# Kernel optimization log

Measured on AMD Instinct MI355X. Metric: run time of the kernel, lower is better.

The kernel has to match this reference:

```python
import jax, jax.numpy as jnp
import numpy as np

B, N, F = 128, 64, 64          # batch, nodes, node features
FE = [2 * F + 1, 256, 256, 96] # edge MLP: fe_in = 2*node_size + num_ef(=1 dist)
FN = [FE[-1] + F, 256, 64]     # node MLP: fe_out + node_size
ALPHA = 0.2

def _lin(key, fan_in, fan_out):
    kw, kb = jax.random.split(key)
    s = 1.0 / np.sqrt(fan_in)
    return (jax.random.normal(kw, (fan_in, fan_out), jnp.float32) * s,
            jax.random.normal(kb, (fan_out,), jnp.float32) * s)

def setup_inputs() -> dict:
    key = jax.random.key(0)
    ks = jax.random.split(key, 6)
    x = jax.random.normal(ks[0], (B, N, F), jnp.float32)
    fe_W0, fe_b0 = _lin(ks[1], FE[0], FE[1])
    fe_W1, fe_b1 = _lin(ks[2], FE[1], FE[2])
    fe_W2, fe_b2 = _lin(ks[3], FE[2], FE[3])
    fn_W0, fn_b0 = _lin(ks[4], FN[0], FN[1])
    fn_W1, fn_b1 = _lin(ks[5], FN[1], FN[2])
    return {"x": x,
            "fe_W0": fe_W0, "fe_b0": fe_b0, "fe_W1": fe_W1, "fe_b1": fe_b1,
            "fe_W2": fe_W2, "fe_b2": fe_b2,
            "fn_W0": fn_W0, "fn_b0": fn_b0, "fn_W1": fn_W1, "fn_b1": fn_b1}

def _lrelu(v):
    return jax.nn.leaky_relu(v, ALPHA)

def reference(x, fe_W0, fe_b0, fe_W1, fe_b1, fe_W2, fe_b2, fn_W0, fn_b0, fn_W1, fn_b1):
    b, n, f = x.shape
    # fully-connected pairwise edge features: x1[b,i,j]=x[b,i], x2[b,i,j]=x[b,j]
    xi = jnp.broadcast_to(x[:, :, None, :], (b, n, n, f))
    xj = jnp.broadcast_to(x[:, None, :, :], (b, n, n, f))
    diffs = xj - xi
    dists = jnp.linalg.norm(diffs + 1e-12, axis=-1, keepdims=True)  # all_ef distance
    A = jnp.concatenate([xi, xj, dists], axis=-1)                   # [B,N,N,2F+1]
    # edge MLP fe (final_linear=False -> leaky relu after every layer)
    h = _lrelu(A @ fe_W0 + fe_b0)
    h = _lrelu(h @ fe_W1 + fe_b1)
    h = _lrelu(h @ fe_W2 + fe_b2)                                   # [B,N,N,96]
    agg = jnp.sum(h, axis=2)                                        # sum over neighbors j
    y = jnp.concatenate([agg, x], axis=-1)                          # [B,N,160]
    # node MLP fn (final_linear=True -> last layer linear)
    y = _lrelu(y @ fn_W0 + fn_b0)
    y = y @ fn_W1 + fn_b1                                           # [B,N,64]
    return y
```

## Files before the change

kernel.cpp:

```cpp
#include <hip/hip_runtime.h>

#define ALPHA 0.2f

typedef __attribute__((ext_vector_type(8))) short short8;
typedef __attribute__((ext_vector_type(4))) float f32x4;
typedef __attribute__((ext_vector_type(2))) unsigned int u32x2;
typedef __attribute__((ext_vector_type(4))) unsigned int u32x4;

__device__ __forceinline__ short f2bf(float f) {
    unsigned u = __builtin_bit_cast(unsigned, f);
    u += 0x7fffu + ((u >> 16) & 1u);
    return (short)(u >> 16);
}
__device__ __forceinline__ unsigned pack2(float a, float b) {
    unsigned ua = __builtin_bit_cast(unsigned, a) + 0x8000u;
    unsigned ub = __builtin_bit_cast(unsigned, b) + 0x8000u;
    return (ua >> 16) | (ub & 0xffff0000u);
}
__device__ __forceinline__ float bf2f(short s) {
    return __builtin_bit_cast(float, ((unsigned)(unsigned short)s) << 16);
}
__device__ __forceinline__ float lrelu(float v) { return fmaxf(v, ALPHA * v); }

__global__ void prep_kernel(const float* __restrict__ feW0, const float* __restrict__ feW1,
                            const float* __restrict__ feW2, const float* __restrict__ fnW0,
                            const float* __restrict__ fnW1,
                            short* __restrict__ W1F, short* __restrict__ W2F,
                            short* __restrict__ W0uvF,
                            short* __restrict__ Wn0T, short* __restrict__ Wn1T)
{
    const int tid = blockIdx.x * blockDim.x + threadIdx.x;
    const int T = gridDim.x * blockDim.x;
    for (int t = tid; t < 65536; t += T) {
        int e = t & 7, lane = (t >> 3) & 63, ks = (t >> 9) & 7, mt = t >> 12;
        int feat = mt * 16 + (lane & 15), k = ks * 32 + (lane >> 4) * 8 + e;
        W1F[t] = f2bf(feW1[k * 256 + feat]);
    }
    for (int t = tid; t < 32768; t += T) {
        int e = t & 7, lane = (t >> 3) & 63, ks = (t >> 9) & 7, mt = t >> 12;
        int feat = mt * 16 + (lane & 15), k = ks * 32 + (lane >> 4) * 8 + e;
        W2F[t] = f2bf(feat < 96 ? feW2[k * 96 + feat] : 0.f);
    }
    for (int t = tid; t < 32768; t += T) {
        int e = t & 7, lane = (t >> 3) & 63, ks = (t >> 9) & 1, mt = t >> 10;
        int feat = mt * 16 + (lane & 15), k = ks * 32 + (lane >> 4) * 8 + e;
        float val = (feat < 256) ? feW0[k * 256 + feat] : feW0[(64 + k) * 256 + (feat - 256)];
        W0uvF[t] = f2bf(val);
    }
    for (int t = tid; t < 256 * 160; t += T) { int n = t / 160, k = t - n * 160; Wn0T[t] = f2bf(fnW0[k * 256 + n]); }
    for (int t = tid; t < 64 * 256; t += T) { int n = t >> 8, k = t & 255; Wn1T[t] = f2bf(fnW1[k * 64 + n]); }
}

__global__ __launch_bounds__(256, 4)
void uv_kernel(const float* __restrict__ x, const short* __restrict__ W0uvF,
               float* __restrict__ u, float* __restrict__ v)
{
    __shared__ __align__(16) short xb[4096];
    const int tid = threadIdx.x;
    const int lane = tid & 63, wid = tid >> 6;
    const int l15 = lane & 15, lg = lane >> 4;
    const int r0 = blockIdx.x * 64;

    for (int t = tid; t < 4096; t += 256) {
        int row = t >> 6;
        int byte = (t * 2) ^ ((row & 7) << 4);
        *(short*)((char*)xb + byte) = f2bf(x[r0 * 64 + t]);
    }
    __syncthreads();

    #pragma unroll
    for (int pair = 0; pair < 4; ++pair) {
        const int mt0 = wid * 8 + pair * 2;
        f32x4 acc[2][4];
        #pragma unroll
        for (int m = 0; m < 2; ++m)
            #pragma unroll
            for (int nt = 0; nt < 4; ++nt) acc[m][nt] = (f32x4){0.f, 0.f, 0.f, 0.f};
        #pragma unroll
        for (int ks = 0; ks < 2; ++ks) {
            short8 a[2], bf[4];
            #pragma unroll
            for (int m = 0; m < 2; ++m)
                a[m] = *(const short8*)&W0uvF[(((mt0 + m) * 2 + ks) * 64 + lane) * 8];
            #pragma unroll
            for (int nt = 0; nt < 4; ++nt) {
                int row = nt * 16 + l15;
                int byte = (row * 128 + (ks * 32 + lg * 8) * 2) ^ ((row & 7) << 4);
                bf[nt] = *(const short8*)((char*)xb + byte);
            }
            #pragma unroll
            for (int m = 0; m < 2; ++m)
                #pragma unroll
                for (int nt = 0; nt < 4; ++nt)
                    acc[m][nt] = __builtin_amdgcn_mfma_f32_16x16x32_bf16(a[m], bf[nt], acc[m][nt], 0, 0, 0);
        }
        #pragma unroll
        for (int m = 0; m < 2; ++m) {
            int feat0 = (mt0 + m) * 16 + lg * 4;
            #pragma unroll
            for (int nt = 0; nt < 4; ++nt) {
                int R = r0 + nt * 16 + l15;
                float* dst = (feat0 < 256) ? &u[R * 256 + feat0] : &v[R * 256 + (feat0 - 256)];
                *(f32x4*)dst = acc[m][nt];
            }
        }
    }
}

__global__ __launch_bounds__(512, 2)
void edge_kernel(const float* __restrict__ x, const float* __restrict__ feW0,
                 const float* __restrict__ b0v, const float* __restrict__ b1v,
                 const float* __restrict__ b2v,
                 const short* __restrict__ W1F, const short* __restrict__ W2F,
                 const float* __restrict__ u, const float* __restrict__ v,
                 float* __restrict__ agg)
{
    __shared__ __align__(16) char smem[119808];
    char* vb = smem;
    char* h0 = smem + 32768;
    char* h1 = smem + 65536;
    float* ub_f = (float*)(smem + 98304);
    float* wd_f = (float*)(smem + 114688);
    float* dist = (float*)(smem + 115712);
    float* xs   = (float*)(smem + 65536);

    const int tid = threadIdx.x;
    const int lane = tid & 63, wid = tid >> 6;
    const int l15 = lane & 15, lg = lane >> 4;
    const int j8 = tid >> 3, p8 = tid & 7;
    const int b = blockIdx.x >> 2, i0 = (blockIdx.x & 3) * 16;

    short8 a1[2][8];
    #pragma unroll
    for (int m = 0; m < 2; ++m)
        #pragma unroll
        for (int ks = 0; ks < 8; ++ks)
            a1[m][ks] = *(const short8*)&W1F[(((wid * 2 + m) * 8 + ks) * 64 + lane) * 8];
    short8 a2[8];
    #pragma unroll
    for (int ks = 0; ks < 8; ++ks)
        a2[ks] = *(const short8*)&W2F[((wid * 8 + ks) * 64 + lane) * 8];
    f32x4 bb1[2];
    bb1[0] = *(const f32x4*)&b1v[wid * 32 + lg * 4];
    bb1[1] = *(const f32x4*)&b1v[wid * 32 + 16 + lg * 4];
    f32x4 bb2 = (f32x4){0.f, 0.f, 0.f, 0.f};
    if (wid < 6) bb2 = *(const f32x4*)&b2v[wid * 16 + lg * 4];

    {
        const float* xb = x + b * 4096;
        *(f32x4*)&xs[j8 * 68 + p8 * 8]     = *(const f32x4*)&xb[j8 * 64 + p8 * 8];
        *(f32x4*)&xs[j8 * 68 + p8 * 8 + 4] = *(const f32x4*)&xb[j8 * 64 + p8 * 8 + 4];
    }
    {
        const float* gv = v + (b * 64 + j8) * 256;
        #pragma unroll
        for (int e = 0; e < 4; ++e) {
            int c0 = p8 * 32 + e * 8;
            f32x4 v0 = *(const f32x4*)&gv[c0];
            f32x4 v1 = *(const f32x4*)&gv[c0 + 4];
            u32x4 pk;
            pk[0] = pack2(v0[0], v0[1]); pk[1] = pack2(v0[2], v0[3]);
            pk[2] = pack2(v1[0], v1[1]); pk[3] = pack2(v1[2], v1[3]);
            *(u32x4*)(vb + ((j8 * 512 + c0 * 2) ^ ((j8 & 7) << 4))) = pk;
        }
    }
    {
        int ii = tid >> 5, c0 = (tid & 31) * 8;
        const float* gu = u + (b * 64 + i0 + ii) * 256 + c0;
        f32x4 u0 = *(const f32x4*)&gu[0];
        f32x4 u1 = *(const f32x4*)&gu[4];
        u0 += *(const f32x4*)&b0v[c0];
        u1 += *(const f32x4*)&b0v[c0 + 4];
        int q = c0 >> 2;
        *(f32x4*)&ub_f[(ii * 64 + (q ^ (q >> 3))) * 4] = u0;
        *(f32x4*)&ub_f[(ii * 64 + ((q + 1) ^ ((q + 1) >> 3))) * 4] = u1;
    }
    if (tid < 64) {
        f32x4 w0 = *(const f32x4*)&feW0[128 * 256 + tid * 4];
        *(f32x4*)&wd_f[(tid ^ (tid >> 3)) * 4] = w0;
    }
    __syncthreads();

    {
        f32x4 xj0 = *(const f32x4*)&xs[j8 * 68 + p8 * 8];
        f32x4 xj1 = *(const f32x4*)&xs[j8 * 68 + p8 * 8 + 4];
        #pragma unroll
        for (int ii = 0; ii < 16; ++ii) {
            const float* xi = &xs[(i0 + ii) * 68 + p8 * 8];
            f32x4 xi0 = *(const f32x4*)&xi[0];
            f32x4 xi1 = *(const f32x4*)&xi[4];
            float ss = 0.f;
            #pragma unroll
            for (int r = 0; r < 4; ++r) {
                float d0 = xj0[r] - xi0[r] + 1e-12f;
                float d1 = xj1[r] - xi1[r] + 1e-12f;
                ss += d0 * d0 + d1 * d1;
            }
            ss += __shfl_xor(ss, 1); ss += __shfl_xor(ss, 2); ss += __shfl_xor(ss, 4);
            if (p8 == 0) dist[ii * 64 + j8] = sqrtf(ss);
        }
    }
    __syncthreads();

    #define BUILD(ii_) do { \
        float dj = dist[(ii_) * 64 + j8]; \
        _Pragma("unroll") \
        for (int e = 0; e < 4; ++e) { \
            int c0 = p8 * 32 + e * 8; \
            int q0 = p8 * 8 + e * 2; \
            short8 vr = *(const short8*)(vb + ((j8 * 512 + c0 * 2) ^ ((j8 & 7) << 4))); \
            f32x4 uu0 = *(const f32x4*)&ub_f[((ii_) * 64 + (q0 ^ p8)) * 4]; \
            f32x4 uu1 = *(const f32x4*)&ub_f[((ii_) * 64 + ((q0 + 1) ^ p8)) * 4]; \
            f32x4 ww0 = *(const f32x4*)&wd_f[(q0 ^ p8) * 4]; \
            f32x4 ww1 = *(const f32x4*)&wd_f[((q0 + 1) ^ p8) * 4]; \
            float t0 = lrelu(uu0[0] + bf2f(vr[0]) + dj * ww0[0]); \
            float t1 = lrelu(uu0[1] + bf2f(vr[1]) + dj * ww0[1]); \
            float t2 = lrelu(uu0[2] + bf2f(vr[2]) + dj * ww0[2]); \
            float t3 = lrelu(uu0[3] + bf2f(vr[3]) + dj * ww0[3]); \
            float t4 = lrelu(uu1[0] + bf2f(vr[4]) + dj * ww1[0]); \
            float t5 = lrelu(uu1[1] + bf2f(vr[5]) + dj * ww1[1]); \
            float t6 = lrelu(uu1[2] + bf2f(vr[6]) + dj * ww1[2]); \
            float t7 = lrelu(uu1[3] + bf2f(vr[7]) + dj * ww1[3]); \
            u32x4 pk; \
            pk[0] = pack2(t0, t1); pk[1] = pack2(t2, t3); \
            pk[2] = pack2(t4, t5); pk[3] = pack2(t6, t7); \
            *(u32x4*)(h0 + ((j8 * 512 + c0 * 2) ^ ((j8 & 7) << 4))) = pk; \
        } \
    } while (0)

    BUILD(0);
    __syncthreads();

    float* aggrow = agg + (b * 64 + i0) * 96;
    for (int ii = 0; ii < 16; ++ii) {
        {
            f32x4 acc[2][4];
            #pragma unroll
            for (int m = 0; m < 2; ++m)
                #pragma unroll
                for (int nt = 0; nt < 4; ++nt) acc[m][nt] = (f32x4){0.f, 0.f, 0.f, 0.f};
            #pragma unroll
            for (int ks = 0; ks < 8; ++ks) {
                short8 bfr[4];
                #pragma unroll
                for (int nt = 0; nt < 4; ++nt) {
                    int j = nt * 16 + l15;
                    bfr[nt] = *(const short8*)(h0 + ((j * 512 + (ks * 32 + lg * 8) * 2) ^ ((j & 7) << 4)));
                }
                #pragma unroll
                for (int m = 0; m < 2; ++m)
                    #pragma unroll
                    for (int nt = 0; nt < 4; ++nt)
                        acc[m][nt] = __builtin_amdgcn_mfma_f32_16x16x32_bf16(a1[m][ks], bfr[nt], acc[m][nt], 0, 0, 0);
            }
            #pragma unroll
            for (int m = 0; m < 2; ++m) {
                int f0 = wid * 32 + m * 16 + lg * 4;
                #pragma unroll
                for (int nt = 0; nt < 4; ++nt) {
                    int j = nt * 16 + l15;
                    float q0 = lrelu(acc[m][nt][0] + bb1[m][0]);
                    float q1 = lrelu(acc[m][nt][1] + bb1[m][1]);
                    float q2 = lrelu(acc[m][nt][2] + bb1[m][2]);
                    float q3 = lrelu(acc[m][nt][3] + bb1[m][3]);
                    u32x2 pv; pv[0] = pack2(q0, q1); pv[1] = pack2(q2, q3);
                    *(u32x2*)(h1 + ((j * 512 + f0 * 2) ^ ((j & 7) << 4))) = pv;
                }
            }
        }
        __syncthreads();
        if (ii < 15) BUILD(ii + 1);
        if (wid < 6) {
            f32x4 acc2[4];
            #pragma unroll
            for (int nt = 0; nt < 4; ++nt) acc2[nt] = (f32x4){0.f, 0.f, 0.f, 0.f};
            #pragma unroll
            for (int ks = 0; ks < 8; ++ks) {
                #pragma unroll
                for (int nt = 0; nt < 4; ++nt) {
                    int j = nt * 16 + l15;
                    short8 bfr = *(const short8*)(h1 + ((j * 512 + (ks * 32 + lg * 8) * 2) ^ ((j & 7) << 4)));
                    acc2[nt] = __builtin_amdgcn_mfma_f32_16x16x32_bf16(a2[ks], bfr, acc2[nt], 0, 0, 0);
                }
            }
            f32x4 s = (f32x4){0.f, 0.f, 0.f, 0.f};
            #pragma unroll
            for (int nt = 0; nt < 4; ++nt)
                #pragma unroll
                for (int r = 0; r < 4; ++r)
                    s[r] += lrelu(acc2[nt][r] + bb2[r]);
            #pragma unroll
            for (int r = 0; r < 4; ++r) {
                float t = s[r];
                t += __shfl_xor(t, 1); t += __shfl_xor(t, 2);
                t += __shfl_xor(t, 4); t += __shfl_xor(t, 8);
                s[r] = t;
            }
            if (l15 == 0) *(f32x4*)&aggrow[ii * 96 + wid * 16 + lg * 4] = s;
        }
        __syncthreads();
    }
    #undef BUILD
}

__global__ __launch_bounds__(256, 2)
void node_kernel(const float* __restrict__ x, const float* __restrict__ agg,
                 const short* __restrict__ Wn0T, const short* __restrict__ Wn1T,
                 const float* __restrict__ bn0, const float* __restrict__ bn1,
                 float* __restrict__ out)
{
    __shared__ short A2[64 * 168];
    __shared__ short H[64 * 264];
    const int tid = threadIdx.x;
    const int lane = tid & 63, wid = tid >> 6;
    const int l15 = lane & 15, lg = lane >> 4;
    const int r0 = blockIdx.x * 64;

    for (int t = tid; t < 64 * 160; t += 256) {
        int j = t / 160, c = t - j * 160;
        float vv = (c < 96) ? agg[(r0 + j) * 96 + c] : x[(r0 + j) * 64 + (c - 96)];
        A2[j * 168 + c] = f2bf(vv);
    }
    __syncthreads();

    {
        f32x4 acc[4][4];
        #pragma unroll
        for (int mt = 0; mt < 4; ++mt)
            #pragma unroll
            for (int nt = 0; nt < 4; ++nt) acc[mt][nt] = (f32x4){0.f, 0.f, 0.f, 0.f};
        const int n0 = wid * 64;
        #pragma unroll
        for (int ks = 0; ks < 5; ++ks) {
            const int k0 = ks * 32 + lg * 8;
            short8 a[4], bf[4];
            #pragma unroll
            for (int mt = 0; mt < 4; ++mt)
                a[mt] = *reinterpret_cast<const short8*>(&A2[(mt * 16 + l15) * 168 + k0]);
            #pragma unroll
            for (int nt = 0; nt < 4; ++nt)
                bf[nt] = *reinterpret_cast<const short8*>(&Wn0T[(n0 + nt * 16 + l15) * 160 + k0]);
            #pragma unroll
            for (int mt = 0; mt < 4; ++mt)
                #pragma unroll
                for (int nt = 0; nt < 4; ++nt)
                    acc[mt][nt] = __builtin_amdgcn_mfma_f32_16x16x32_bf16(a[mt], bf[nt], acc[mt][nt], 0, 0, 0);
        }
        #pragma unroll
        for (int nt = 0; nt < 4; ++nt) {
            const int col = n0 + nt * 16 + l15;
            const float bv = bn0[col];
            #pragma unroll
            for (int mt = 0; mt < 4; ++mt)
                #pragma unroll
                for (int r = 0; r < 4; ++r)
                    H[(mt * 16 + lg * 4 + r) * 264 + col] = f2bf(lrelu(acc[mt][nt][r] + bv));
        }
    }
    __syncthreads();

    {
        f32x4 acc[4];
        #pragma unroll
        for (int mt = 0; mt < 4; ++mt) acc[mt] = (f32x4){0.f, 0.f, 0.f, 0.f};
        #pragma unroll
        for (int ks = 0; ks < 8; ++ks) {
            const int k0 = ks * 32 + lg * 8;
            short8 bf = *reinterpret_cast<const short8*>(&Wn1T[(wid * 16 + l15) * 256 + k0]);
            #pragma unroll
            for (int mt = 0; mt < 4; ++mt) {
                short8 a = *reinterpret_cast<const short8*>(&H[(mt * 16 + l15) * 264 + k0]);
                acc[mt] = __builtin_amdgcn_mfma_f32_16x16x32_bf16(a, bf, acc[mt], 0, 0, 0);
            }
        }
        const int col = wid * 16 + l15;
        const float bv = bn1[col];
        #pragma unroll
        for (int mt = 0; mt < 4; ++mt)
            #pragma unroll
            for (int r = 0; r < 4; ++r)
                out[(r0 + mt * 16 + lg * 4 + r) * 64 + col] = acc[mt][r] + bv;
    }
}

extern "C" void kernel_launch(void* const* d_in, const int* in_sizes, int n_in,
                              void* d_out, int out_size, void* d_ws, size_t ws_size,
                              hipStream_t stream) {
    (void)in_sizes; (void)n_in; (void)out_size; (void)ws_size;
    const float* x    = (const float*)d_in[0];
    const float* feW0 = (const float*)d_in[1];
    const float* feb0 = (const float*)d_in[2];
    const float* feW1 = (const float*)d_in[3];
    const float* feb1 = (const float*)d_in[4];
    const float* feW2 = (const float*)d_in[5];
    const float* feb2 = (const float*)d_in[6];
    const float* fnW0 = (const float*)d_in[7];
    const float* fnb0 = (const float*)d_in[8];
    const float* fnW1 = (const float*)d_in[9];
    const float* fnb1 = (const float*)d_in[10];

    char* ws = (char*)d_ws;
    short* W1F   = (short*)(ws + 0);
    short* W2F   = (short*)(ws + 131072);
    short* W0uvF = (short*)(ws + 196608);
    short* Wn0T  = (short*)(ws + 262144);
    short* Wn1T  = (short*)(ws + 344064);
    float* agg   = (float*)(ws + 376832);
    float* u     = (float*)(ws + 3522560);
    float* v     = (float*)(ws + 11911168);

    hipLaunchKernelGGL(prep_kernel, dim3(64), dim3(256), 0, stream,
                       feW0, feW1, feW2, fnW0, fnW1, W1F, W2F, W0uvF, Wn0T, Wn1T);
    hipLaunchKernelGGL(uv_kernel, dim3(128), dim3(256), 0, stream,
                       x, W0uvF, u, v);
    hipLaunchKernelGGL(edge_kernel, dim3(512), dim3(512), 0, stream,
                       x, feW0, feb0, feb1, feb2, W1F, W2F, u, v, agg);
    hipLaunchKernelGGL(node_kernel, dim3(128), dim3(256), 0, stream,
                       x, agg, Wn0T, Wn1T, fnb0, fnb1, (float*)d_out);
}
```

Measured before the change: 163.4 us.

## Re-tile edge MLP waves as 4 feature groups by 2 neighbor halves

Changes how the 8 waves split the edge-MLP layer-1 and layer-2 GEMMs. Each wave now covers 64 output features by 32 neighbors, where before it covered 32 features by all 64 neighbors, and all 8 waves now work on layer 2 instead of only 6. Layer-2 partial neighbor sums are combined through a small shared buffer, and each aggregated row is written one iteration late. Biases move to shared memory, and s_setprio is raised around the MFMA bursts. The aim is better wave balance and higher B-operand reuse in layer 2, at the cost of more A-fragment registers, some shared memory, and wasted MFMA work on the zero-padded features 96-127.

```diff
diff --git a/kernel.cpp b/kernel.cpp
--- a/kernel.cpp
+++ b/kernel.cpp
@@ -115,36 +115,37 @@
                  const float* __restrict__ u, const float* __restrict__ v,
                  float* __restrict__ agg)
 {
-    __shared__ __align__(16) char smem[119808];
+    __shared__ __align__(16) char smem[122368];
     char* vb = smem;
     char* h0 = smem + 32768;
     char* h1 = smem + 65536;
     float* ub_f = (float*)(smem + 98304);
     float* wd_f = (float*)(smem + 114688);
     float* dist = (float*)(smem + 115712);
+    float* part = (float*)(smem + 119808);
+    float* bb1s = (float*)(smem + 120832);
+    float* bb2s = (float*)(smem + 121856);
     float* xs   = (float*)(smem + 65536);
 
     const int tid = threadIdx.x;
     const int lane = tid & 63, wid = tid >> 6;
     const int l15 = lane & 15, lg = lane >> 4;
     const int j8 = tid >> 3, p8 = tid & 7;
+    const int fw = wid & 3, jh = wid >> 2;
     const int b = blockIdx.x >> 2, i0 = (blockIdx.x & 3) * 16;
 
-    short8 a1[2][8];
+    short8 a1[4][8];
+    #pragma unroll
+    for (int m = 0; m < 4; ++m)
+        #pragma unroll
+        for (int ks = 0; ks < 8; ++ks)
+            a1[m][ks] = *(const short8*)&W1F[(((fw * 4 + m) * 8 + ks) * 64 + lane) * 8];
+    short8 a2[2][8];
     #pragma unroll
     for (int m = 0; m < 2; ++m)
         #pragma unroll
         for (int ks = 0; ks < 8; ++ks)
-            a1[m][ks] = *(const short8*)&W1F[(((wid * 2 + m) * 8 + ks) * 64 + lane) * 8];
-    short8 a2[8];
-    #pragma unroll
-    for (int ks = 0; ks < 8; ++ks)
-        a2[ks] = *(const short8*)&W2F[((wid * 8 + ks) * 64 + lane) * 8];
-    f32x4 bb1[2];
-    bb1[0] = *(const f32x4*)&b1v[wid * 32 + lg * 4];
-    bb1[1] = *(const f32x4*)&b1v[wid * 32 + 16 + lg * 4];
-    f32x4 bb2 = (f32x4){0.f, 0.f, 0.f, 0.f};
-    if (wid < 6) bb2 = *(const f32x4*)&b2v[wid * 16 + lg * 4];
+            a2[m][ks] = *(const short8*)&W2F[(((fw * 2 + m) * 8 + ks) * 64 + lane) * 8];
 
     {
         const float* xb = x + b * 4096;
@@ -172,13 +173,15 @@
         u0 += *(const f32x4*)&b0v[c0];
         u1 += *(const f32x4*)&b0v[c0 + 4];
         int q = c0 >> 2;
-        *(f32x4*)&ub_f[(ii * 64 + (q ^ (q >> 3))) * 4] = u0;
-        *(f32x4*)&ub_f[(ii * 64 + ((q + 1) ^ ((q + 1) >> 3))) * 4] = u1;
+        *(f32x4*)&ub_f[(q ^ (q >> 3)) * 4 + ii * 256] = u0;
+        *(f32x4*)&ub_f[((q + 1) ^ ((q + 1) >> 3)) * 4 + ii * 256] = u1;
     }
     if (tid < 64) {
         f32x4 w0 = *(const f32x4*)&feW0[128 * 256 + tid * 4];
         *(f32x4*)&wd_f[(tid ^ (tid >> 3)) * 4] = w0;
     }
+    if (tid < 256) bb1s[tid] = b1v[tid];
+    if (tid >= 256 && tid < 384) bb2s[tid - 256] = (tid - 256 < 96) ? b2v[tid - 256] : 0.f;
     __syncthreads();
 
     {
@@ -209,8 +212,8 @@
             int c0 = p8 * 32 + e * 8; \
             int q0 = p8 * 8 + e * 2; \
             short8 vr = *(const short8*)(vb + ((j8 * 512 + c0 * 2) ^ ((j8 & 7) << 4))); \
-            f32x4 uu0 = *(const f32x4*)&ub_f[((ii_) * 64 + (q0 ^ p8)) * 4]; \
-            f32x4 uu1 = *(const f32x4*)&ub_f[((ii_) * 64 + ((q0 + 1) ^ p8)) * 4]; \
+            f32x4 uu0 = *(const f32x4*)&ub_f[(q0 ^ p8) * 4 + (ii_) * 256]; \
+            f32x4 uu1 = *(const f32x4*)&ub_f[((q0 + 1) ^ p8) * 4 + (ii_) * 256]; \
             f32x4 ww0 = *(const f32x4*)&wd_f[(q0 ^ p8) * 4]; \
             f32x4 ww1 = *(const f32x4*)&wd_f[((q0 + 1) ^ p8) * 4]; \
             float t0 = lrelu(uu0[0] + bf2f(vr[0]) + dj * ww0[0]); \
@@ -233,36 +236,42 @@
 
     float* aggrow = agg + (b * 64 + i0) * 96;
     for (int ii = 0; ii < 16; ++ii) {
+        if (ii > 0 && tid < 96)
+            aggrow[(ii - 1) * 96 + tid] = part[tid] + part[128 + tid];
         {
-            f32x4 acc[2][4];
-            #pragma unroll
-            for (int m = 0; m < 2; ++m)
-                #pragma unroll
-                for (int nt = 0; nt < 4; ++nt) acc[m][nt] = (f32x4){0.f, 0.f, 0.f, 0.f};
+            f32x4 acc[4][2];
+            #pragma unroll
+            for (int m = 0; m < 4; ++m) {
+                acc[m][0] = (f32x4){0.f, 0.f, 0.f, 0.f};
+                acc[m][1] = (f32x4){0.f, 0.f, 0.f, 0.f};
+            }
             #pragma unroll
             for (int ks = 0; ks < 8; ++ks) {
-                short8 bfr[4];
-                #pragma unroll
-                for (int nt = 0; nt < 4; ++nt) {
-                    int j = nt * 16 + l15;
+                short8 bfr[2];
+                #pragma unroll
+                for (int nt = 0; nt < 2; ++nt) {
+                    int j = jh * 32 + nt * 16 + l15;
                     bfr[nt] = *(const short8*)(h0 + ((j * 512 + (ks * 32 + lg * 8) * 2) ^ ((j & 7) << 4)));
                 }
-                #pragma unroll
-                for (int m = 0; m < 2; ++m)
+                __builtin_amdgcn_s_setprio(1);
+                #pragma unroll
+                for (int m = 0; m < 4; ++m)
                     #pragma unroll
-                    for (int nt = 0; nt < 4; ++nt)
+                    for (int nt = 0; nt < 2; ++nt)
                         acc[m][nt] = __builtin_amdgcn_mfma_f32_16x16x32_bf16(a1[m][ks], bfr[nt], acc[m][nt], 0, 0, 0);
-            }
-            #pragma unroll
-            for (int m = 0; m < 2; ++m) {
-                int f0 = wid * 32 + m * 16 + lg * 4;
-                #pragma unroll
-                for (int nt = 0; nt < 4; ++nt) {
-                    int j = nt * 16 + l15;
-                    float q0 = lrelu(acc[m][nt][0] + bb1[m][0]);
-                    float q1 = lrelu(acc[m][nt][1] + bb1[m][1]);
-                    float q2 = lrelu(acc[m][nt][2] + bb1[m][2]);
-                    float q3 = lrelu(acc[m][nt][3] + bb1[m][3]);
+                __builtin_amdgcn_s_setprio(0);
+            }
+            #pragma unroll
+            for (int m = 0; m < 4; ++m) {
+                int f0 = fw * 64 + m * 16 + lg * 4;
+                f32x4 bb = *(const f32x4*)&bb1s[f0];
+                #pragma unroll
+                for (int nt = 0; nt < 2; ++nt) {
+                    int j = jh * 32 + nt * 16 + l15;
+                    float q0 = lrelu(acc[m][nt][0] + bb[0]);
+                    float q1 = lrelu(acc[m][nt][1] + bb[1]);
+                    float q2 = lrelu(acc[m][nt][2] + bb[2]);
+                    float q3 = lrelu(acc[m][nt][3] + bb[3]);
                     u32x2 pv; pv[0] = pack2(q0, q1); pv[1] = pack2(q2, q3);
                     *(u32x2*)(h1 + ((j * 512 + f0 * 2) ^ ((j & 7) << 4))) = pv;
                 }
@@ -270,36 +279,48 @@
         }
         __syncthreads();
         if (ii < 15) BUILD(ii + 1);
-        if (wid < 6) {
-            f32x4 acc2[4];
-            #pragma unroll
-            for (int nt = 0; nt < 4; ++nt) acc2[nt] = (f32x4){0.f, 0.f, 0.f, 0.f};
+        {
+            f32x4 acc2[2][2];
+            acc2[0][0] = (f32x4){0.f,0.f,0.f,0.f}; acc2[0][1] = (f32x4){0.f,0.f,0.f,0.f};
+            acc2[1][0] = (f32x4){0.f,0.f,0.f,0.f}; acc2[1][1] = (f32x4){0.f,0.f,0.f,0.f};
             #pragma unroll
             for (int ks = 0; ks < 8; ++ks) {
-                #pragma unroll
-                for (int nt = 0; nt < 4; ++nt) {
-                    int j = nt * 16 + l15;
-                    short8 bfr = *(const short8*)(h1 + ((j * 512 + (ks * 32 + lg * 8) * 2) ^ ((j & 7) << 4)));
-                    acc2[nt] = __builtin_amdgcn_mfma_f32_16x16x32_bf16(a2[ks], bfr, acc2[nt], 0, 0, 0);
+                short8 bfr[2];
+                #pragma unroll
+                for (int nt = 0; nt < 2; ++nt) {
+                    int j = jh * 32 + nt * 16 + l15;
+                    bfr[nt] = *(const short8*)(h1 + ((j * 512 + (ks * 32 + lg * 8) * 2) ^ ((j & 7) << 4)));
                 }
-            }
-            f32x4 s = (f32x4){0.f, 0.f, 0.f, 0.f};
-            #pragma unroll
-            for (int nt = 0; nt < 4; ++nt)
+                __builtin_amdgcn_s_setprio(1);
+                #pragma unroll
+                for (int m = 0; m < 2; ++m)
+                    #pragma unroll
+                    for (int nt = 0; nt < 2; ++nt)
+                        acc2[m][nt] = __builtin_amdgcn_mfma_f32_16x16x32_bf16(a2[m][ks], bfr[nt], acc2[m][nt], 0, 0, 0);
+                __builtin_amdgcn_s_setprio(0);
+            }
+            #pragma unroll
+            for (int m = 0; m < 2; ++m) {
+                int f0 = fw * 32 + m * 16 + lg * 4;
+                f32x4 bb = *(const f32x4*)&bb2s[f0];
+                f32x4 s;
                 #pragma unroll
                 for (int r = 0; r < 4; ++r)
-                    s[r] += lrelu(acc2[nt][r] + bb2[r]);
-            #pragma unroll
-            for (int r = 0; r < 4; ++r) {
-                float t = s[r];
-                t += __shfl_xor(t, 1); t += __shfl_xor(t, 2);
-                t += __shfl_xor(t, 4); t += __shfl_xor(t, 8);
-                s[r] = t;
-            }
-            if (l15 == 0) *(f32x4*)&aggrow[ii * 96 + wid * 16 + lg * 4] = s;
+                    s[r] = lrelu(acc2[m][0][r] + bb[r]) + lrelu(acc2[m][1][r] + bb[r]);
+                #pragma unroll
+                for (int r = 0; r < 4; ++r) {
+                    float t = s[r];
+                    t += __shfl_xor(t, 1); t += __shfl_xor(t, 2);
+                    t += __shfl_xor(t, 4); t += __shfl_xor(t, 8);
+                    s[r] = t;
+                }
+                if (l15 == 0) *(f32x4*)&part[jh * 128 + f0] = s;
+            }
         }
         __syncthreads();
     }
+    if (tid < 96)
+        aggrow[15 * 96 + tid] = part[tid] + part[128 + tid];
     #undef BUILD
 }
 
```

Measured after the change: 230.8 us. 41.3% more time.

## Shrink edge kernel LDS by reading v from global and storing u as bf16

Applied to the files above, without the earlier changes.

The per-block v tile is no longer staged in LDS as bf16; BUILD now reads v directly from global memory (likely L2/L1 resident) in fp32. The u+bias rows are stored as packed bf16 instead of fp32, and the layer-1/2 biases move from registers into LDS to ease register pressure. Shared memory drops from about 117 KB to about 78 KB, which may allow more blocks per CU. In exchange, every BUILD step issues repeated global loads of v, and u is rounded to bf16 earlier.

```diff
diff --git a/kernel.cpp b/kernel.cpp
--- a/kernel.cpp
+++ b/kernel.cpp
@@ -115,20 +115,22 @@
                  const float* __restrict__ u, const float* __restrict__ v,
                  float* __restrict__ agg)
 {
-    __shared__ __align__(16) char smem[119808];
-    char* vb = smem;
-    char* h0 = smem + 32768;
-    char* h1 = smem + 65536;
-    float* ub_f = (float*)(smem + 98304);
-    float* wd_f = (float*)(smem + 114688);
-    float* dist = (float*)(smem + 115712);
-    float* xs   = (float*)(smem + 65536);
+    __shared__ __align__(16) char smem[80384];
+    char* h0 = smem;
+    char* h1 = smem + 32768;
+    short* ub_b = (short*)(smem + 65536);
+    float* wd_f = (float*)(smem + 73728);
+    float* dist = (float*)(smem + 74752);
+    float* bb1s = (float*)(smem + 78848);
+    float* bb2s = (float*)(smem + 79872);
+    float* xs   = (float*)(smem + 32768);
 
     const int tid = threadIdx.x;
     const int lane = tid & 63, wid = tid >> 6;
     const int l15 = lane & 15, lg = lane >> 4;
     const int j8 = tid >> 3, p8 = tid & 7;
     const int b = blockIdx.x >> 2, i0 = (blockIdx.x & 3) * 16;
+    const float* vbase = v + (size_t)b * 64 * 256;
 
     short8 a1[2][8];
     #pragma unroll
@@ -139,12 +141,7 @@
     short8 a2[8];
     #pragma unroll
     for (int ks = 0; ks < 8; ++ks)
-        a2[ks] = *(const short8*)&W2F[((wid * 8 + ks) * 64 + lane) * 8];
-    f32x4 bb1[2];
-    bb1[0] = *(const f32x4*)&b1v[wid * 32 + lg * 4];
-    bb1[1] = *(const f32x4*)&b1v[wid * 32 + 16 + lg * 4];
-    f32x4 bb2 = (f32x4){0.f, 0.f, 0.f, 0.f};
-    if (wid < 6) bb2 = *(const f32x4*)&b2v[wid * 16 + lg * 4];
+        a2[ks] = *(const short8*)&W2F[((min(wid, 5) * 8 + ks) * 64 + lane) * 8];
 
     {
         const float* xb = x + b * 4096;
@@ -152,33 +149,22 @@
         *(f32x4*)&xs[j8 * 68 + p8 * 8 + 4] = *(const f32x4*)&xb[j8 * 64 + p8 * 8 + 4];
     }
     {
-        const float* gv = v + (b * 64 + j8) * 256;
-        #pragma unroll
-        for (int e = 0; e < 4; ++e) {
-            int c0 = p8 * 32 + e * 8;
-            f32x4 v0 = *(const f32x4*)&gv[c0];
-            f32x4 v1 = *(const f32x4*)&gv[c0 + 4];
-            u32x4 pk;
-            pk[0] = pack2(v0[0], v0[1]); pk[1] = pack2(v0[2], v0[3]);
-            pk[2] = pack2(v1[0], v1[1]); pk[3] = pack2(v1[2], v1[3]);
-            *(u32x4*)(vb + ((j8 * 512 + c0 * 2) ^ ((j8 & 7) << 4))) = pk;
-        }
-    }
-    {
         int ii = tid >> 5, c0 = (tid & 31) * 8;
-        const float* gu = u + (b * 64 + i0 + ii) * 256 + c0;
-        f32x4 u0 = *(const f32x4*)&gu[0];
-        f32x4 u1 = *(const f32x4*)&gu[4];
+        f32x4 u0 = *(const f32x4*)&u[(b * 64 + i0 + ii) * 256 + c0];
+        f32x4 u1 = *(const f32x4*)&u[(b * 64 + i0 + ii) * 256 + c0 + 4];
         u0 += *(const f32x4*)&b0v[c0];
         u1 += *(const f32x4*)&b0v[c0 + 4];
-        int q = c0 >> 2;
-        *(f32x4*)&ub_f[(ii * 64 + (q ^ (q >> 3))) * 4] = u0;
-        *(f32x4*)&ub_f[(ii * 64 + ((q + 1) ^ ((q + 1) >> 3))) * 4] = u1;
+        u32x4 pk;
+        pk[0] = pack2(u0[0], u0[1]); pk[1] = pack2(u0[2], u0[3]);
+        pk[2] = pack2(u1[0], u1[1]); pk[3] = pack2(u1[2], u1[3]);
+        *(u32x4*)&ub_b[ii * 256 + c0] = pk;
     }
     if (tid < 64) {
         f32x4 w0 = *(const f32x4*)&feW0[128 * 256 + tid * 4];
-        *(f32x4*)&wd_f[(tid ^ (tid >> 3)) * 4] = w0;
-    }
+        *(f32x4*)&wd_f[tid * 4] = w0;
+    }
+    if (tid < 256) bb1s[tid] = b1v[tid];
+    else if (tid < 352) bb2s[tid - 256] = b2v[tid - 256];
     __syncthreads();
 
     {
@@ -204,23 +190,23 @@
 
     #define BUILD(ii_) do { \
         float dj = dist[(ii_) * 64 + j8]; \
+        const float* gv = vbase + j8 * 256 + p8 * 32; \
         _Pragma("unroll") \
         for (int e = 0; e < 4; ++e) { \
             int c0 = p8 * 32 + e * 8; \
-            int q0 = p8 * 8 + e * 2; \
-            short8 vr = *(const short8*)(vb + ((j8 * 512 + c0 * 2) ^ ((j8 & 7) << 4))); \
-            f32x4 uu0 = *(const f32x4*)&ub_f[((ii_) * 64 + (q0 ^ p8)) * 4]; \
-            f32x4 uu1 = *(const f32x4*)&ub_f[((ii_) * 64 + ((q0 + 1) ^ p8)) * 4]; \
-            f32x4 ww0 = *(const f32x4*)&wd_f[(q0 ^ p8) * 4]; \
-            f32x4 ww1 = *(const f32x4*)&wd_f[((q0 + 1) ^ p8) * 4]; \
-            float t0 = lrelu(uu0[0] + bf2f(vr[0]) + dj * ww0[0]); \
-            float t1 = lrelu(uu0[1] + bf2f(vr[1]) + dj * ww0[1]); \
-            float t2 = lrelu(uu0[2] + bf2f(vr[2]) + dj * ww0[2]); \
-            float t3 = lrelu(uu0[3] + bf2f(vr[3]) + dj * ww0[3]); \
-            float t4 = lrelu(uu1[0] + bf2f(vr[4]) + dj * ww1[0]); \
-            float t5 = lrelu(uu1[1] + bf2f(vr[5]) + dj * ww1[1]); \
-            float t6 = lrelu(uu1[2] + bf2f(vr[6]) + dj * ww1[2]); \
-            float t7 = lrelu(uu1[3] + bf2f(vr[7]) + dj * ww1[3]); \
+            f32x4 va = *(const f32x4*)&gv[e * 8]; \
+            f32x4 vb4 = *(const f32x4*)&gv[e * 8 + 4]; \
+            short8 ur = *(const short8*)&ub_b[(ii_) * 256 + c0]; \
+            f32x4 ww0 = *(const f32x4*)&wd_f[c0]; \
+            f32x4 ww1 = *(const f32x4*)&wd_f[c0 + 4]; \
+            float t0 = lrelu(bf2f(ur[0]) + va[0] + dj * ww0[0]); \
+            float t1 = lrelu(bf2f(ur[1]) + va[1] + dj * ww0[1]); \
+            float t2 = lrelu(bf2f(ur[2]) + va[2] + dj * ww0[2]); \
+            float t3 = lrelu(bf2f(ur[3]) + va[3] + dj * ww0[3]); \
+            float t4 = lrelu(bf2f(ur[4]) + vb4[0] + dj * ww1[0]); \
+            float t5 = lrelu(bf2f(ur[5]) + vb4[1] + dj * ww1[1]); \
+            float t6 = lrelu(bf2f(ur[6]) + vb4[2] + dj * ww1[2]); \
+            float t7 = lrelu(bf2f(ur[7]) + vb4[3] + dj * ww1[3]); \
             u32x4 pk; \
             pk[0] = pack2(t0, t1); pk[1] = pack2(t2, t3); \
             pk[2] = pack2(t4, t5); pk[3] = pack2(t6, t7); \
@@ -256,13 +242,14 @@
             #pragma unroll
             for (int m = 0; m < 2; ++m) {
                 int f0 = wid * 32 + m * 16 + lg * 4;
+                f32x4 bb = *(const f32x4*)&bb1s[f0];
                 #pragma unroll
                 for (int nt = 0; nt < 4; ++nt) {
                     int j = nt * 16 + l15;
-                    float q0 = lrelu(acc[m][nt][0] + bb1[m][0]);
-                    float q1 = lrelu(acc[m][nt][1] + bb1[m][1]);
-                    float q2 = lrelu(acc[m][nt][2] + bb1[m][2]);
-                    float q3 = lrelu(acc[m][nt][3] + bb1[m][3]);
+                    float q0 = lrelu(acc[m][nt][0] + bb[0]);
+                    float q1 = lrelu(acc[m][nt][1] + bb[1]);
+                    float q2 = lrelu(acc[m][nt][2] + bb[2]);
+                    float q3 = lrelu(acc[m][nt][3] + bb[3]);
                     u32x2 pv; pv[0] = pack2(q0, q1); pv[1] = pack2(q2, q3);
                     *(u32x2*)(h1 + ((j * 512 + f0 * 2) ^ ((j & 7) << 4))) = pv;
                 }
@@ -283,12 +270,14 @@
                     acc2[nt] = __builtin_amdgcn_mfma_f32_16x16x32_bf16(a2[ks], bfr, acc2[nt], 0, 0, 0);
                 }
             }
+            const int f0 = wid * 16 + lg * 4;
+            f32x4 bb = *(const f32x4*)&bb2s[f0];
             f32x4 s = (f32x4){0.f, 0.f, 0.f, 0.f};
             #pragma unroll
             for (int nt = 0; nt < 4; ++nt)
                 #pragma unroll
                 for (int r = 0; r < 4; ++r)
-                    s[r] += lrelu(acc2[nt][r] + bb2[r]);
+                    s[r] += lrelu(acc2[nt][r] + bb[r]);
             #pragma unroll
             for (int r = 0; r < 4; ++r) {
                 float t = s[r];
@@ -296,7 +285,7 @@
                 t += __shfl_xor(t, 4); t += __shfl_xor(t, 8);
                 s[r] = t;
             }
-            if (l15 == 0) *(f32x4*)&aggrow[ii * 96 + wid * 16 + lg * 4] = s;
+            if (l15 == 0) *(f32x4*)&aggrow[ii * 96 + f0] = s;
         }
         __syncthreads();
     }
```

After: 198.0 us. 21.2% more time.
